# Optimization experiments

Measured on AMD Instinct MI355X. Metric: run time of the kernel, lower is better.

Reference implementation:

```python
import math
import jax, jax.numpy as jnp
import numpy as np

# ---- hard-coded constants from the source module ----
T_H = 1.5; M = 60; DT = T_H / M; SQDT = math.sqrt(DT)
ALPHA = 0.8; RHO = 0.3; SQ1MR2 = math.sqrt(1.0 - RHO * RHO)
GAMMA = 5.0; KAPPA_Y = 1.2; LB_W = 1e-3
R = 0.02; SIGMA = 0.2; SIGMA_Y = 0.3; THETA_Y = 0.0; PI_CAP = 2.0
RPTS = 128       # sub_batch (one accumulation iteration)
REPEATS = 128    # total repeats == sub_batch -> single loop pass
N_PTS = 32       # number of eval states
HID = 64


def setup_inputs():
    key = jax.random.key(0)
    ks = jax.random.split(key, 8)
    W = 0.8 + 0.4 * jax.random.uniform(ks[0], (N_PTS, 1), jnp.float32)   # W0_range
    Y = -1.0 + 2.0 * jax.random.uniform(ks[1], (N_PTS, 1), jnp.float32)  # Y0_range
    TmT = jnp.full((N_PTS, 1), T_H, jnp.float32)
    B = RPTS * N_PTS
    # [sim(+/-), draw(z1/z2), step, path, 1] -- fresh noise per antithetic branch, as in torch
    noise = jax.random.normal(ks[2], (2, 2, M, B, 1), jnp.float32)
    w1 = 0.1 * jax.random.normal(ks[3], (3, HID), jnp.float32)
    b1 = jnp.zeros((HID,), jnp.float32)
    w2 = 0.1 * jax.random.normal(ks[4], (HID, HID), jnp.float32)
    b2 = jnp.zeros((HID,), jnp.float32)
    w3 = 0.1 * jax.random.normal(ks[5], (HID, 1), jnp.float32)
    b3 = jnp.zeros((1,), jnp.float32)
    return {"W": W, "TmT": TmT, "Y": Y, "noise": noise,
            "w1": w1, "b1": b1, "w2": w2, "b2": b2, "w3": w3, "b3": b3}


def _policy(params, W, TmT, Y):
    w1, b1, w2, b2, w3, b3 = params
    x = jnp.concatenate([W, TmT, Y], axis=-1)          # [B,3]
    h = jnp.tanh(x @ w1 + b1)
    h = jnp.tanh(h @ w2 + b2)
    return h @ w3 + b3                                 # [B,1]


def _simulate(params, W0, Y0, z1, z2, anti):
    """60-step Euler-Maruyama; returns CRRA utility U(W_T), shape [B,1]."""
    logW = jnp.log(jnp.clip(W0, LB_W, None))
    TmT0 = jnp.full_like(W0, T_H)

    def step(carry, zs):
        logW, Y, TmT = carry
        z1s, z2s = zs
        pi = _policy(params, jnp.exp(logW), TmT, Y)
        zW = anti * z1s
        zY = anti * (RHO * z1s + SQ1MR2 * z2s)
        drift = R + pi * (SIGMA * ALPHA * Y)
        var = (pi * SIGMA) ** 2
        logW = logW + (drift - 0.5 * var) * DT + pi * SIGMA * SQDT * zW
        Y = Y + KAPPA_Y * (THETA_Y - Y) * DT + SIGMA_Y * SQDT * zY
        logW = jnp.log(jnp.clip(jnp.exp(logW), LB_W, None))
        return (logW, Y, TmT - DT), None

    (logW, _, _), _ = jax.lax.scan(step, (logW, Y0, TmT0), (z1, z2))
    W_T = jnp.exp(logW)
    return W_T ** (1.0 - GAMMA) / (1.0 - GAMMA)        # gamma != 1


def reference(W, TmT, Y, noise, w1, b1, w2, b2, w3, b3):
    params = (w1, b1, w2, b2, w3, b3)
    n = W.shape[0]
    Wd = jax.lax.stop_gradient(W)   # forward detaches W, Y
    Yd = jax.lax.stop_gradient(Y)
    W0 = jnp.tile(Wd, (RPTS, 1))    # [B,1]
    Y0 = jnp.tile(Yd, (RPTS, 1))
    z1p, z2p = noise[0, 0], noise[0, 1]
    z1m, z2m = noise[1, 0], noise[1, 1]

    def f(W0_, Y0_):
        U = 0.5 * (_simulate(params, W0_, Y0_, z1p, z2p, 1.0)
                   + _simulate(params, W0_, Y0_, z1m, z2m, -1.0))
        # U_avg.sum() as in torch: mean over rpts, sum over eval points
        return jnp.sum(jnp.mean(U.reshape(RPTS, n), axis=0))

    lam_full = jax.grad(f, 0)(W0, Y0)                  # [B,1]

    def g(W0_, Y0_):
        # lam.view(rpts,n,1).mean(0).sum() == sum(lam_full)/rpts
        return jnp.sum(jax.grad(f, 0)(W0_, Y0_)) / RPTS

    dW_full, dY_full = jax.grad(g, (0, 1))(W0, Y0)     # [B,1] each

    inv = 1.0 / REPEATS   # faithful to source accumulation scaling
    lam = lam_full.reshape(RPTS, n, 1).mean(0) * inv
    dlamW = dW_full.reshape(RPTS, n, 1).mean(0) * inv
    dlamY = dY_full.reshape(RPTS, n, 1).mean(0) * inv

    # project_pmp
    mu_minus_r = SIGMA * (ALPHA * Yd)
    coeff = -1.0 / (Wd * dlamW + 1e-8)
    myo = coeff * (lam * (mu_minus_r / SIGMA ** 2))
    hedge = coeff * (SIGMA * RHO * SIGMA_Y * dlamY / SIGMA ** 2)
    return jnp.clip(myo + hedge, -PI_CAP, PI_CAP)      # [n,1]
```

## Files before the change

kernel.cpp:

```cpp
#include <hip/hip_runtime.h>
#include <math.h>

#define HID    64
#define MSTEPS 60
#define NPTS   32
#define RPTSC  128
#define BTOT   (RPTSC*NPTS)
#define NSIM   (2*BTOT)
#define NWAVE  (NSIM/2)

#define C_DT     0.025f
#define C_SQDT   0.15811388300841897f
#define C_ALPHA  0.8f
#define C_RHO    0.3f
#define C_SQ1MR2 0.9539392014169456f
#define C_KAPPA  1.2f
#define C_R      0.02f
#define C_SIGMA  0.2f
#define C_SIGY   0.3f
#define C_LBW    1e-3f
#define C_LOGLBW -6.907755279f
#define C_2L2E   2.8853900817779268f

#define WAVE_LDS 3584
#define A_ROW    144
#define OFF_DV   2304
#define OFF_DA   3328

typedef _Float16 half8 __attribute__((ext_vector_type(8)));
typedef float    f32x4 __attribute__((ext_vector_type(4)));
typedef _Float16 h2    __attribute__((ext_vector_type(2)));

__device__ __forceinline__ float rlanef(float v, int l) {
    return __int_as_float(__builtin_amdgcn_readlane(__float_as_int(v), l));
}
template <int OFF>
__device__ __forceinline__ float swz(float v) {
    return __int_as_float(__builtin_amdgcn_ds_swizzle(__float_as_int(v), OFF));
}
__device__ __forceinline__ f32x4 MFMA(half8 a, half8 b, f32x4 c) {
    return __builtin_amdgcn_mfma_f32_16x16x32_f16(a, b, c, 0, 0, 0);
}
__device__ __forceinline__ int pk16(float a, float b) {
    return __builtin_bit_cast(int, __builtin_amdgcn_cvt_pkrtz(a, b));
}
__device__ __forceinline__ h2 pk2(float a, float b) {
    return __builtin_bit_cast(h2, __builtin_amdgcn_cvt_pkrtz(a, b));
}
__device__ __forceinline__ h2 permh(unsigned s0, unsigned s1, unsigned sel) {
    return __builtin_bit_cast(h2, __builtin_amdgcn_perm(s0, s1, sel));
}
__device__ __forceinline__ float tanh_fast(float xs) {
    return 1.0f - 2.0f * __builtin_amdgcn_rcpf(__builtin_amdgcn_exp2f(xs) + 1.0f);
}

__global__ __launch_bounds__(256, 4) void sim_kernel(
    const float* __restrict__ noise,
    const float* __restrict__ w1, const float* __restrict__ b1,
    const float* __restrict__ w2, const float* __restrict__ b2,
    const float* __restrict__ w3, const float* __restrict__ b3,
    const float* __restrict__ Wp, const float* __restrict__ Yp,
    float* __restrict__ sd)
{
    __shared__ __align__(16) char smem[4 * WAVE_LDS];
    const int lane = threadIdx.x & 63;
    const int quad = lane >> 4;
    const int mrow = lane & 15;
    const int par  = lane >> 5;
    char* wb = smem + (threadIdx.x >> 6) * WAVE_LDS;

    const int w = __builtin_amdgcn_readfirstlane(
        (int)((blockIdx.x * blockDim.x + threadIdx.x) >> 6));
    const int simb = w >> 11;
    const int pg   = 2*(w & 2047) + par;
    const int i    = pg & (NPTS - 1);

    const float cW  = w1[lane];
    const float cT  = w1[HID + lane];
    const float cYw = w1[2*HID + lane];
    const float b1k = b1[lane];
    const float b2k = b2[lane];
    const float b3v = b3[0];
    const float cW_s  = cW  * C_2L2E;
    const float cT_s  = cT  * C_2L2E;
    const float cYw_s = cYw * C_2L2E;
    const float b1_s  = b1k * C_2L2E;
    const float b2_s  = b2k * C_2L2E;
    const h2 cWh  = pk2(cW, cW);
    const h2 cYwh = pk2(cYw, cYw);
    const h2 cW2m = pk2(-2.0f*cW*cW,  -2.0f*cW*cW);
    const h2 cWYm = pk2(-2.0f*cW*cYw, -2.0f*cW*cYw);
    const h2 hone = {(_Float16)1.0f,  (_Float16)1.0f};
    const h2 m2h  = {(_Float16)-2.0f, (_Float16)-2.0f};

    half8 B00, B01, B02, B03, B10, B11, B12, B13, W30, W31;
    {
        half8 h;
        #define LOADB(dst, q, t) \
            { for (int j = 0; j < 8; ++j) \
                h[j] = (_Float16)w2[((q)*32 + quad*8 + j)*HID + (t)*16 + mrow]; \
              dst = h; }
        LOADB(B00, 0, 0) LOADB(B01, 0, 1) LOADB(B02, 0, 2) LOADB(B03, 0, 3)
        LOADB(B10, 1, 0) LOADB(B11, 1, 1) LOADB(B12, 1, 2) LOADB(B13, 1, 3)
        #undef LOADB
        for (int j = 0; j < 8; ++j) h[j] = (_Float16)w3[0*32 + quad*8 + j];
        W30 = h;
        for (int j = 0; j < 8; ++j) h[j] = (_Float16)w3[1*32 + quad*8 + j];
        W31 = h;
    }

    for (int off = lane*4; off < 16*A_ROW; off += 256)
        *(float*)(wb + off) = 0.0f;

    _Float16* swp = (_Float16*)(wb + lane*2);
    char* arp0 = wb + mrow*A_ROW + quad*16;

    const float* zp1 = noise + (size_t)(simb*2 + 0) * MSTEPS * BTOT + pg;
    const float* zp2 = noise + (size_t)(simb*2 + 1) * MSTEPS * BTOT + pg;

    const float anti = simb ? -1.0f : 1.0f;
    const float ksa  = C_SIGMA * C_ALPHA;
    const float ks2  = C_SIGMA * C_SIGMA;
    const float ksn  = anti * C_SIGMA * C_SQDT;
    const float kFy  = ksa * C_DT;
    const float ksd  = ks2 * C_DT;
    const float kv   = 0.5f * ks2 * C_DT;
    const float kRdt = C_R * C_DT;
    const float ky1  = anti * C_SIGY * C_SQDT * C_RHO;
    const float ky2  = anti * C_SIGY * C_SQDT * C_SQ1MR2;
    const float cYfac = 1.0f - C_KAPPA * C_DT;

    const float W0 = Wp[i];
    float L   = __logf(fmaxf(W0, C_LBW));
    float W   = __expf(L);
    float Yv  = Yp[i];
    float tmt = 1.5f;
    float gW  = 1.0f / W0;
    float hWW = -gW * gW;
    float gY  = 0.0f, hWY = 0.0f;
    float cYt = 1.0f;

    #pragma unroll 1
    for (int m = 0; m < MSTEPS; ++m) {
        asm volatile("" : "+v"(B00), "+v"(B01), "+v"(B02), "+v"(B03),
                          "+v"(B10), "+v"(B11), "+v"(B12), "+v"(B13),
                          "+v"(W30), "+v"(W31));

        const float z1 = zp1[(size_t)m * BTOT];
        const float z2 = zp2[(size_t)m * BTOT];

        const float Wb0 = rlanef(W, 0),  Wb1 = rlanef(W, 32);
        const float Yb0 = rlanef(Yv, 0), Yb1 = rlanef(Yv, 32);

        const float base1s = fmaf(tmt, cT_s, b1_s);
        {
            const float t10 = tanh_fast(fmaf(Wb0, cW_s, fmaf(Yb0, cYw_s, base1s)));
            const float t11 = tanh_fast(fmaf(Wb1, cW_s, fmaf(Yb1, cYw_s, base1s)));
            const h2 tp  = pk2(t10, t11);
            const h2 dpp = hone - tp * tp;
            const h2 ddq = tp * dpp;
            const h2 r1 = dpp * cWh;
            const h2 r2 = dpp * cYwh;
            const h2 r3 = ddq * cW2m;
            const h2 r4 = ddq * cWYm;
            swp[0*72] = tp.x;  swp[8*72]  = tp.y;
            swp[1*72] = r1.x;  swp[9*72]  = r1.y;
            swp[2*72] = r2.x;  swp[10*72] = r2.y;
            swp[3*72] = r3.x;  swp[11*72] = r3.y;
            swp[4*72] = r4.x;  swp[12*72] = r4.y;
        }

        half8 af0 = __builtin_bit_cast(half8, *(const f32x4*)arp0);
        half8 af1 = __builtin_bit_cast(half8, *(const f32x4*)(arp0 + 64));

        f32x4 acc[4];
        const f32x4 zz = {0.f, 0.f, 0.f, 0.f};
        acc[0] = MFMA(af1, B10, MFMA(af0, B00, zz));
        acc[1] = MFMA(af1, B11, MFMA(af0, B01, zz));
        acc[2] = MFMA(af1, B12, MFMA(af0, B02, zz));
        acc[3] = MFMA(af1, B13, MFMA(af0, B03, zz));

        {
            const int p = quad >> 1;
            if (!(quad & 1)) {
                #pragma unroll
                for (int t = 0; t < 4; ++t) {
                    int2 v;
                    v.x = pk16(acc[t].x, acc[t].y);
                    v.y = pk16(acc[t].z, acc[t].w);
                    *(int2*)(wb + OFF_DV + ((t*16 + mrow) << 4) + (p << 3)) = v;
                }
            } else {
                #pragma unroll
                for (int t = 0; t < 4; ++t)
                    *(_Float16*)(wb + OFF_DA + ((t*16 + mrow) << 2) + (p << 1)) =
                        (_Float16)acc[t].x;
            }
        }

        const f32x4 dvv = *(const f32x4*)(wb + OFF_DV + lane*16);
        const h2 awyp   = *(const h2*)(wb + OFF_DA + lane*4);
        {
            const unsigned q0 = __builtin_bit_cast(unsigned, dvv.x);
            const unsigned q1 = __builtin_bit_cast(unsigned, dvv.y);
            const unsigned q2 = __builtin_bit_cast(unsigned, dvv.z);
            const unsigned q3 = __builtin_bit_cast(unsigned, dvv.w);
            const h2 a0p  = permh(q2, q0, 0x05040100);
            const h2 aWp  = permh(q2, q0, 0x07060302);
            const h2 aYp  = permh(q3, q1, 0x05040100);
            const h2 aWWp = permh(q3, q1, 0x07060302);

            const float t20 = tanh_fast(fmaf((float)a0p.x, C_2L2E, b2_s));
            const float t21 = tanh_fast(fmaf((float)a0p.y, C_2L2E, b2_s));
            const h2 t2p = pk2(t20, t21);
            const h2 d2p = hone - t2p * t2p;
            const h2 qp  = (m2h * (t2p * d2p)) * aWp;
            const h2 s1 = d2p * aWp;
            const h2 s2 = d2p * aYp;
            const h2 s3 = qp * aWp + d2p * aWWp;
            const h2 s4 = qp * aYp + d2p * awyp;
            swp[0*72] = t2p.x; swp[8*72]  = t2p.y;
            swp[1*72] = s1.x;  swp[9*72]  = s1.y;
            swp[2*72] = s2.x;  swp[10*72] = s2.y;
            swp[3*72] = s3.x;  swp[11*72] = s3.y;
            swp[4*72] = s4.x;  swp[12*72] = s4.y;
        }

        half8 bf0 = __builtin_bit_cast(half8, *(const f32x4*)arp0);
        half8 bf1 = __builtin_bit_cast(half8, *(const f32x4*)(arp0 + 64));
        f32x4 acc4 = MFMA(bf1, W31, MFMA(bf0, W30, zz));

        const float pi  = swz<0x0000>(acc4.x) + b3v;
        const float pW  = swz<0x0000>(acc4.y);
        const float pY  = swz<0x0000>(acc4.z);
        const float pWW = swz<0x0000>(acc4.w);
        const float pWY = swz<0x0200>(acc4.x);

        const float Sn    = ksn * z1;
        const float say   = ksa * Yv;
        const float G     = fmaf(-ks2, pi, say);
        const float GdtSn = fmaf(G, C_DT, Sn);

        const float w2v  = W * W;
        const float piL  = pW * W;
        const float piLL = fmaf(pWW, w2v, piL);
        const float piY  = pY;
        const float piLY = pWY * W;

        const float pi2  = pi * pi;
        const float Lnew = fmaf(pi, fmaf(say, C_DT, Sn),
                                fmaf(-kv, pi2, L + kRdt));

        const float F_L  = fmaf(piL, GdtSn, 1.0f);
        const float F_Y  = fmaf(piY, GdtSn, kFy * pi);
        const float piL2 = piL * piL;
        const float F_LL = fmaf(piLL, GdtSn, -(ksd * piL2));
        const float F_LY = fmaf(piLY, GdtSn, piL * fmaf(-ksd, piY, kFy));

        const float gW2  = gW * gW;
        const float hWWn = fmaf(F_LL, gW2, F_L * hWW);
        const float hWYn = fmaf(F_LL, gW * gY,
                                fmaf(F_LY, gW * cYt, F_L * hWY));
        const float gWn  = F_L * gW;
        const float gYn  = fmaf(F_Y, cYt, F_L * gY);

        Yv  = fmaf(ky2, z2, fmaf(ky1, z1, cYfac * Yv));
        cYt *= cYfac;

        const float We   = __expf(Lnew);
        const bool  clip = (We < C_LBW);
        L   = clip ? C_LOGLBW : Lnew;
        W   = clip ? C_LBW    : We;
        gW  = clip ? 0.0f : gWn;
        gY  = clip ? 0.0f : gYn;
        hWW = clip ? 0.0f : hWWn;
        hWY = clip ? 0.0f : hWYn;
        tmt -= C_DT;
    }

    const float E   = __expf(-4.0f * L);
    const float d1  = E * gW;
    const float d2v = fmaf(-4.0f * E, gW * gW, E * hWW);
    const float d3v = fmaf(-4.0f * E, gW * gY, E * hWY);

    if ((lane & 31) == 0) {
        const int branch = simb * BTOT + pg;
        sd[         branch] = 0.5f * d1;
        sd[  NSIM + branch] = 0.5f * d2v;
        sd[2*NSIM + branch] = 0.5f * d3v;
    }
}

__global__ __launch_bounds__(512) void proj_kernel(
    const float* __restrict__ sd,
    const float* __restrict__ Wp,
    const float* __restrict__ Yp,
    float* __restrict__ out)
{
    __shared__ float red[3 * 512];
    const int tid = threadIdx.x;
    const int i = tid & 31;
    const int c = tid >> 5;
    float lam = 0.f, dW = 0.f, dY = 0.f;
    #pragma unroll 4
    for (int jj = 0; jj < 16; ++jj) {
        const int idx = i + ((jj*16 + c) << 5);
        lam += sd[idx];
        dW  += sd[NSIM + idx];
        dY  += sd[2*NSIM + idx];
    }
    red[tid] = lam; red[512 + tid] = dW; red[1024 + tid] = dY;
    __syncthreads();
    if (tid < NPTS) {
        float l = 0.f, w = 0.f, y = 0.f;
        #pragma unroll
        for (int c2 = 0; c2 < 16; ++c2) {
            l += red[c2*32 + i];
            w += red[512 + c2*32 + i];
            y += red[1024 + c2*32 + i];
        }
        l *= (1.0f / 2097152.0f);
        w *= (1.0f / 268435456.0f);
        y *= (1.0f / 268435456.0f);
        const float Wv = Wp[i], Yv = Yp[i];
        const float mmr   = C_SIGMA * (C_ALPHA * Yv);
        const float sig2  = C_SIGMA * C_SIGMA;
        const float coeff = -1.0f / (Wv * w + 1e-8f);
        const float myo   = coeff * (l * (mmr / sig2));
        const float hedge = coeff * (C_SIGMA * C_RHO * C_SIGY * y / sig2);
        float v = myo + hedge;
        v = fminf(fmaxf(v, -2.0f), 2.0f);
        out[i] = v;
    }
}

extern "C" void kernel_launch(void* const* d_in, const int* in_sizes, int n_in,
                              void* d_out, int out_size, void* d_ws, size_t ws_size,
                              hipStream_t stream) {
    const float* Wp    = (const float*)d_in[0];
    const float* Yp    = (const float*)d_in[2];
    const float* noise = (const float*)d_in[3];
    const float* w1    = (const float*)d_in[4];
    const float* b1    = (const float*)d_in[5];
    const float* w2    = (const float*)d_in[6];
    const float* b2    = (const float*)d_in[7];
    const float* w3    = (const float*)d_in[8];
    const float* b3    = (const float*)d_in[9];
    float* out = (float*)d_out;
    float* sd  = (float*)d_ws;

    hipLaunchKernelGGL(sim_kernel, dim3(NWAVE/4), dim3(256), 0, stream,
                       noise, w1, b1, w2, b2, w3, b3, Wp, Yp, sd);
    hipLaunchKernelGGL(proj_kernel, dim3(1), dim3(512), 0, stream, sd, Wp, Yp, out);
}
```

Before: 163.0 us.

## Fuse projection into sim kernel, prefetch noise, keep layer-1 outputs in fp32 LDS

Removes the separate projection launch: the last block to finish, found with a global atomic counter, does the reduction and PMP projection. The next step's noise values are loaded one iteration ahead to hide global load latency. MFMA accumulators are now staged in LDS as fp32 instead of packed fp16, which drops the pack/perm instructions but doubles LDS traffic and per-wave LDS size. The counter uses modulo NBLK, so it works across repeated launches without a reset, provided the workspace starts at zero.

```diff
diff --git a/kernel.cpp b/kernel.cpp
--- a/kernel.cpp
+++ b/kernel.cpp
@@ -8,6 +8,7 @@
 #define BTOT   (RPTSC*NPTS)
 #define NSIM   (2*BTOT)
 #define NWAVE  (NSIM/2)
+#define NBLK   (NWAVE/4)
 
 #define C_DT     0.025f
 #define C_SQDT   0.15811388300841897f
@@ -22,10 +23,10 @@
 #define C_LOGLBW -6.907755279f
 #define C_2L2E   2.8853900817779268f
 
-#define WAVE_LDS 3584
+#define WAVE_LDS 4864
 #define A_ROW    144
 #define OFF_DV   2304
-#define OFF_DA   3328
+#define OFF_DA   4352
 
 typedef _Float16 half8 __attribute__((ext_vector_type(8)));
 typedef float    f32x4 __attribute__((ext_vector_type(4)));
@@ -41,14 +42,8 @@
 __device__ __forceinline__ f32x4 MFMA(half8 a, half8 b, f32x4 c) {
     return __builtin_amdgcn_mfma_f32_16x16x32_f16(a, b, c, 0, 0, 0);
 }
-__device__ __forceinline__ int pk16(float a, float b) {
-    return __builtin_bit_cast(int, __builtin_amdgcn_cvt_pkrtz(a, b));
-}
 __device__ __forceinline__ h2 pk2(float a, float b) {
     return __builtin_bit_cast(h2, __builtin_amdgcn_cvt_pkrtz(a, b));
-}
-__device__ __forceinline__ h2 permh(unsigned s0, unsigned s1, unsigned sel) {
-    return __builtin_bit_cast(h2, __builtin_amdgcn_perm(s0, s1, sel));
 }
 __device__ __forceinline__ float tanh_fast(float xs) {
     return 1.0f - 2.0f * __builtin_amdgcn_rcpf(__builtin_amdgcn_exp2f(xs) + 1.0f);
@@ -60,9 +55,11 @@
     const float* __restrict__ w2, const float* __restrict__ b2,
     const float* __restrict__ w3, const float* __restrict__ b3,
     const float* __restrict__ Wp, const float* __restrict__ Yp,
-    float* __restrict__ sd)
+    float* __restrict__ sd, unsigned int* __restrict__ cnt,
+    float* __restrict__ out)
 {
     __shared__ __align__(16) char smem[4 * WAVE_LDS];
+    __shared__ int lastf;
     const int lane = threadIdx.x & 63;
     const int quad = lane >> 4;
     const int mrow = lane & 15;
@@ -140,14 +137,19 @@
     float gY  = 0.0f, hWY = 0.0f;
     float cYt = 1.0f;
 
+    float z1c = zp1[0];
+    float z2c = zp2[0];
+
     #pragma unroll 1
     for (int m = 0; m < MSTEPS; ++m) {
         asm volatile("" : "+v"(B00), "+v"(B01), "+v"(B02), "+v"(B03),
                           "+v"(B10), "+v"(B11), "+v"(B12), "+v"(B13),
                           "+v"(W30), "+v"(W31));
 
-        const float z1 = zp1[(size_t)m * BTOT];
-        const float z2 = zp2[(size_t)m * BTOT];
+        const float z1 = z1c, z2 = z2c;
+        const int mn = (m + 1 < MSTEPS) ? m + 1 : m;
+        z1c = zp1[(size_t)mn * BTOT];
+        z2c = zp2[(size_t)mn * BTOT];
 
         const float Wb0 = rlanef(W, 0),  Wb1 = rlanef(W, 32);
         const float Yb0 = rlanef(Yv, 0), Yb1 = rlanef(Yv, 32);
@@ -184,34 +186,26 @@
             const int p = quad >> 1;
             if (!(quad & 1)) {
                 #pragma unroll
-                for (int t = 0; t < 4; ++t) {
-                    int2 v;
-                    v.x = pk16(acc[t].x, acc[t].y);
-                    v.y = pk16(acc[t].z, acc[t].w);
-                    *(int2*)(wb + OFF_DV + ((t*16 + mrow) << 4) + (p << 3)) = v;
-                }
+                for (int t = 0; t < 4; ++t)
+                    *(f32x4*)(wb + OFF_DV + ((t*16 + mrow) << 5) + (p << 4)) = acc[t];
             } else {
                 #pragma unroll
                 for (int t = 0; t < 4; ++t)
-                    *(_Float16*)(wb + OFF_DA + ((t*16 + mrow) << 2) + (p << 1)) =
-                        (_Float16)acc[t].x;
+                    *(float*)(wb + OFF_DA + ((t*16 + mrow) << 3) + (p << 2)) =
+                        acc[t].x;
             }
         }
 
-        const f32x4 dvv = *(const f32x4*)(wb + OFF_DV + lane*16);
-        const h2 awyp   = *(const h2*)(wb + OFF_DA + lane*4);
+        const f32x4 v0 = *(const f32x4*)(wb + OFF_DV + (lane << 5));
+        const f32x4 v1 = *(const f32x4*)(wb + OFF_DV + (lane << 5) + 16);
+        const float2 aw = *(const float2*)(wb + OFF_DA + (lane << 3));
         {
-            const unsigned q0 = __builtin_bit_cast(unsigned, dvv.x);
-            const unsigned q1 = __builtin_bit_cast(unsigned, dvv.y);
-            const unsigned q2 = __builtin_bit_cast(unsigned, dvv.z);
-            const unsigned q3 = __builtin_bit_cast(unsigned, dvv.w);
-            const h2 a0p  = permh(q2, q0, 0x05040100);
-            const h2 aWp  = permh(q2, q0, 0x07060302);
-            const h2 aYp  = permh(q3, q1, 0x05040100);
-            const h2 aWWp = permh(q3, q1, 0x07060302);
-
-            const float t20 = tanh_fast(fmaf((float)a0p.x, C_2L2E, b2_s));
-            const float t21 = tanh_fast(fmaf((float)a0p.y, C_2L2E, b2_s));
+            const h2 aWp  = pk2(v0.y, v1.y);
+            const h2 aYp  = pk2(v0.z, v1.z);
+            const h2 aWWp = pk2(v0.w, v1.w);
+            const h2 awyp = pk2(aw.x, aw.y);
+            const float t20 = tanh_fast(fmaf(v0.x, C_2L2E, b2_s));
+            const float t21 = tanh_fast(fmaf(v1.x, C_2L2E, b2_s));
             const h2 t2p = pk2(t20, t21);
             const h2 d2p = hone - t2p * t2p;
             const h2 qp  = (m2h * (t2p * d2p)) * aWp;
@@ -289,48 +283,51 @@
         sd[  NSIM + branch] = 0.5f * d2v;
         sd[2*NSIM + branch] = 0.5f * d3v;
     }
-}
-
-__global__ __launch_bounds__(512) void proj_kernel(
-    const float* __restrict__ sd,
-    const float* __restrict__ Wp,
-    const float* __restrict__ Yp,
-    float* __restrict__ out)
-{
-    __shared__ float red[3 * 512];
-    const int tid = threadIdx.x;
-    const int i = tid & 31;
-    const int c = tid >> 5;
-    float lam = 0.f, dW = 0.f, dY = 0.f;
-    #pragma unroll 4
-    for (int jj = 0; jj < 16; ++jj) {
-        const int idx = i + ((jj*16 + c) << 5);
-        lam += sd[idx];
-        dW  += sd[NSIM + idx];
-        dY  += sd[2*NSIM + idx];
-    }
-    red[tid] = lam; red[512 + tid] = dW; red[1024 + tid] = dY;
+
+    __threadfence();
     __syncthreads();
-    if (tid < NPTS) {
-        float l = 0.f, w = 0.f, y = 0.f;
-        #pragma unroll
-        for (int c2 = 0; c2 < 16; ++c2) {
-            l += red[c2*32 + i];
-            w += red[512 + c2*32 + i];
-            y += red[1024 + c2*32 + i];
-        }
-        l *= (1.0f / 2097152.0f);
-        w *= (1.0f / 268435456.0f);
-        y *= (1.0f / 268435456.0f);
-        const float Wv = Wp[i], Yv = Yp[i];
-        const float mmr   = C_SIGMA * (C_ALPHA * Yv);
-        const float sig2  = C_SIGMA * C_SIGMA;
-        const float coeff = -1.0f / (Wv * w + 1e-8f);
-        const float myo   = coeff * (l * (mmr / sig2));
-        const float hedge = coeff * (C_SIGMA * C_RHO * C_SIGY * y / sig2);
-        float v = myo + hedge;
-        v = fminf(fmaxf(v, -2.0f), 2.0f);
-        out[i] = v;
+    if (threadIdx.x == 0) {
+        const unsigned old = atomicAdd(cnt, 1u);
+        lastf = ((old & (NBLK - 1u)) == (NBLK - 1u)) ? 1 : 0;
+    }
+    __syncthreads();
+    if (lastf) {
+        __threadfence();
+        float* red = (float*)smem;
+        const int tid = threadIdx.x;
+        const int ii  = tid & 31;
+        const int c   = tid >> 5;
+        float lam = 0.f, dWs = 0.f, dYs = 0.f;
+        #pragma unroll 4
+        for (int jj = 0; jj < 32; ++jj) {
+            const int idx = ii + ((jj*8 + c) << 5);
+            lam += sd[idx];
+            dWs += sd[NSIM + idx];
+            dYs += sd[2*NSIM + idx];
+        }
+        red[tid] = lam; red[256 + tid] = dWs; red[512 + tid] = dYs;
+        __syncthreads();
+        if (tid < NPTS) {
+            float l = 0.f, wv = 0.f, y = 0.f;
+            #pragma unroll
+            for (int c2 = 0; c2 < 8; ++c2) {
+                l  += red[c2*32 + ii];
+                wv += red[256 + c2*32 + ii];
+                y  += red[512 + c2*32 + ii];
+            }
+            l  *= (1.0f / 2097152.0f);
+            wv *= (1.0f / 268435456.0f);
+            y  *= (1.0f / 268435456.0f);
+            const float Wv = Wp[ii], Yvv = Yp[ii];
+            const float mmr   = C_SIGMA * (C_ALPHA * Yvv);
+            const float sig2  = C_SIGMA * C_SIGMA;
+            const float coeff = -1.0f / (Wv * wv + 1e-8f);
+            const float myo   = coeff * (l * (mmr / sig2));
+            const float hedge = coeff * (C_SIGMA * C_RHO * C_SIGY * y / sig2);
+            float v = myo + hedge;
+            v = fminf(fmaxf(v, -2.0f), 2.0f);
+            out[ii] = v;
+        }
     }
 }
 
@@ -348,8 +345,8 @@
     const float* b3    = (const float*)d_in[9];
     float* out = (float*)d_out;
     float* sd  = (float*)d_ws;
-
-    hipLaunchKernelGGL(sim_kernel, dim3(NWAVE/4), dim3(256), 0, stream,
-                       noise, w1, b1, w2, b2, w3, b3, Wp, Yp, sd);
-    hipLaunchKernelGGL(proj_kernel, dim3(1), dim3(512), 0, stream, sd, Wp, Yp, out);
-}
+    unsigned int* cnt = (unsigned int*)((char*)d_ws + 3*NSIM*sizeof(float));
+
+    hipLaunchKernelGGL(sim_kernel, dim3(NBLK), dim3(256), 0, stream,
+                       noise, w1, b1, w2, b2, w3, b3, Wp, Yp, sd, cnt, out);
+}
```

Result: slower. 226.0 us (+38.6%).
